# Optimization experiments

Hardware: AMD Instinct MI355X
Metric: run time of the kernel (lower is better)

The kernel has to match this reference:

```python
import jax, jax.numpy as jnp
import numpy as np

B, C, H, W = 16, 64, 64, 64  # z_e shape; C == embedding_dim
K = 1024                     # num_embeddings
COMMITMENT_COST = 0.25
EPS = 1e-5


def setup_inputs() -> dict:
    key = jax.random.key(0)
    k1, k2 = jax.random.split(key)
    z_e = jax.random.normal(k1, (B, C, H, W), dtype=jnp.float32)
    # codebook init ~ U(-1/D, 1/D) as in the torch module
    emb_w = jax.random.uniform(k2, (K, C), dtype=jnp.float32, minval=-1.0 / C, maxval=1.0 / C)
    return {"z_e": z_e, "emb_w": emb_w}


def reference(z_e, emb_w):
    orig_dtype = z_e.dtype
    b, c, h, w = z_e.shape
    z = z_e.astype(jnp.float32)
    # per-channel std over (batch, h, w); computed under no_grad in torch -> stop_gradient
    std = jax.lax.stop_gradient(
        jnp.clip(jnp.std(z, axis=(0, 2, 3), keepdims=True, ddof=1), EPS, None)
    )
    z = z / std                                        # [b,c,h,w]
    zf = z.transpose(0, 2, 3, 1).reshape(-1, c)        # [N, c]
    ew = emb_w.astype(jnp.float32)                     # [K, c]
    # squared euclidean distances: ||z||^2 - 2 z.e + ||e||^2  -> [N, K]
    d = (
        jnp.sum(zf * zf, axis=1, keepdims=True)
        - 2.0 * (zf @ ew.T)
        + jnp.sum(ew * ew, axis=1)
    )
    idx = jnp.argmin(d, axis=1)                        # [N]
    z_q = ew[idx].reshape(b, h, w, c).transpose(0, 3, 1, 2)  # [b,c,h,w]
    z_sg = jax.lax.stop_gradient(z)
    commitment = COMMITMENT_COST * jnp.mean((z_sg - z_q) ** 2)
    codebook = jnp.mean((z_sg - z_q) ** 2)             # eval-mode codebook loss
    vq_loss = commitment + codebook
    z_q_st = (z + jax.lax.stop_gradient(z_q - z)).astype(orig_dtype)
    n_tokens = idx.shape[0]
    counts = jnp.zeros((K,), dtype=jnp.float32).at[idx].add(1.0)
    avg_probs = counts / n_tokens
    perplexity = jnp.exp(-jnp.sum(avg_probs * jnp.log(jnp.clip(avg_probs, 1e-10, None))))
    indices = idx.reshape(b, h, w)
    return z_q_st, vq_loss, perplexity, indices
```

## Files before the change

### kernel.cpp

```cpp
#include <hip/hip_runtime.h>
#include <math.h>
#include <float.h>

#define HW 4096
#define CHW 262144
#define NTOK 65536
#define NELEM 4194304

#define WS_LOSS 0
#define WS_STD  512
#define WS_EE   576
#define WS_E2   1600

#define EPSM 1.5e-4f

typedef __attribute__((ext_vector_type(8))) short bf16x8;
typedef __attribute__((ext_vector_type(4))) float f32x4;

__device__ __forceinline__ unsigned short f2bf(float x) {
  unsigned u = __float_as_uint(x);
  u += 0x7FFFu + ((u >> 16) & 1u);
  return (unsigned short)(u >> 16);
}
__device__ __forceinline__ float bf2f(unsigned short h) {
  return __uint_as_float(((unsigned)h) << 16);
}
__device__ __forceinline__ void gload_lds16(const unsigned short* g, unsigned short* l) {
  __builtin_amdgcn_global_load_lds(
      (const __attribute__((address_space(1))) unsigned int*)g,
      (__attribute__((address_space(3))) unsigned int*)l, 16, 0, 0);
}

__global__ __launch_bounds__(1024) void k_pre(const float* __restrict__ z,
                                              const float* __restrict__ emb,
                                              float* __restrict__ stdv,
                                              unsigned short* __restrict__ e2g,
                                              float* __restrict__ eeg) {
  __shared__ double rs[16], rs2[16];
  int tid = threadIdx.x;
  int blk = blockIdx.x;
  if (blk < 64) {
    int c = blk;
    double s = 0.0, s2 = 0.0;
    const float* base = z + c * HW;
    #pragma unroll 4
    for (int jj = 0; jj < 16; ++jj) {
      int f = tid + (jj << 10);
      int b = f >> 10, off4 = f & 1023;
      float4 v = *(const float4*)(base + (size_t)b * CHW + (off4 << 2));
      s  += (double)v.x + (double)v.y + (double)v.z + (double)v.w;
      s2 += (double)v.x * v.x + (double)v.y * v.y + (double)v.z * v.z + (double)v.w * v.w;
    }
    for (int o = 32; o > 0; o >>= 1) {
      s += __shfl_down(s, o, 64);
      s2 += __shfl_down(s2, o, 64);
    }
    int wv = tid >> 6, ln = tid & 63;
    if (ln == 0) { rs[wv] = s; rs2[wv] = s2; }
    __syncthreads();
    if (tid == 0) {
      double S = 0.0, S2 = 0.0;
      #pragma unroll
      for (int w = 0; w < 16; ++w) { S += rs[w]; S2 += rs2[w]; }
      const double N = (double)NTOK;
      double var = (S2 - S * S / N) / (N - 1.0);
      float sd = (float)sqrt(var);
      stdv[c] = fmaxf(sd, 1e-5f);
    }
  } else {
    int ct = blk - 64;
    int k0 = ct << 6;
    int code = tid >> 4, c4 = tid & 15;
    float4 v = *(const float4*)(emb + (size_t)((k0 + code) << 6) + (c4 << 2));
    unsigned short h0 = f2bf(v.x), h1 = f2bf(v.y), h2 = f2bf(v.z), h3 = f2bf(v.w);
    unsigned short l0 = f2bf(v.x - bf2f(h0)), l1 = f2bf(v.y - bf2f(h1));
    unsigned short l2 = f2bf(v.z - bf2f(h2)), l3 = f2bf(v.w - bf2f(h3));
    int jL = (c4 >> 1) & 3;
    int e = (c4 & 1) << 2;
    int cH = code >> 4, cL = code & 15;
    size_t base = (size_t)ct * 8192 + cH * 512 + jL * 128 + cL * 8 + e;
    int jHh = c4 >> 3;
    *(uint2*)(e2g + base + (size_t)jHh * 2048) =
        make_uint2((unsigned)h0 | ((unsigned)h1 << 16), (unsigned)h2 | ((unsigned)h3 << 16));
    *(uint2*)(e2g + base + (size_t)(2 + jHh) * 2048) =
        make_uint2((unsigned)l0 | ((unsigned)l1 << 16), (unsigned)l2 | ((unsigned)l3 << 16));
    if (tid < 64) {
      const float* er = emb + (size_t)((k0 + tid) << 6);
      float s = 0.f;
      #pragma unroll
      for (int c = 0; c < 64; ++c) s = fmaf(er[c], er[c], s);
      eeg[k0 + tid] = s;
    }
  }
}

__global__ __launch_bounds__(256, 2) void k_vq(
    const float* __restrict__ z_e, const float* __restrict__ emb,
    const float* __restrict__ stdv, const float* __restrict__ eeg,
    const unsigned short* __restrict__ e2g,
    float* __restrict__ out_zq, float* __restrict__ out_idx,
    float* __restrict__ loss_part) {
  __shared__ unsigned short A2[16384];
  __shared__ unsigned short B2[16384];
  float* mbd = (float*)A2;
  float* msec = (float*)A2 + 256;
  int*   mbk = (int*)A2 + 512;
  int*   skf = (int*)A2 + 768;
  int*   ambList = (int*)A2 + 896;
  int*   ambN = (int*)A2 + 1024;
  float* sred = (float*)A2 + 1028;
  float* zf   = (float*)A2 + 1040;
  float* fbd4 = (float*)A2 + 1104;
  int*   fbk4 = (int*)A2 + 1108;

  int tid = threadIdx.x;
  int lane = tid & 63;
  int wv = tid >> 6;
  int blk = blockIdx.x;
  int b = blk >> 5;
  int s0 = (blk & 31) << 7;

  {
    int tok = tid >> 1, half = tid & 1;
    const float* zsrc = z_e + (size_t)b * CHW + (size_t)(half << 5) * HW + s0 + tok;
    unsigned hw_[16], lw_[16];
    #pragma unroll
    for (int cc = 0; cc < 32; ++cc) {
      float v = zsrc[(size_t)cc * HW] / stdv[(half << 5) + cc];
      unsigned short h = f2bf(v);
      unsigned short l = f2bf(v - bf2f(h));
      if (cc & 1) { hw_[cc >> 1] |= ((unsigned)h) << 16; lw_[cc >> 1] |= ((unsigned)l) << 16; }
      else        { hw_[cc >> 1] = h;                    lw_[cc >> 1] = l; }
    }
    int tH = tok >> 4, tL = tok & 15;
    int base = tH * 512 + tL * 8;
    #pragma unroll
    for (int jj = 0; jj < 4; ++jj) {
      *(uint4*)(A2 + half * 4096 + base + jj * 128) =
          make_uint4(hw_[4 * jj], hw_[4 * jj + 1], hw_[4 * jj + 2], hw_[4 * jj + 3]);
      *(uint4*)(A2 + (2 + half) * 4096 + base + jj * 128) =
          make_uint4(lw_[4 * jj], lw_[4 * jj + 1], lw_[4 * jj + 2], lw_[4 * jj + 3]);
    }
  }

  int quad = lane >> 4, l15 = lane & 15;
  int wt = wv >> 1, wc = wv & 1;

  float bd[16], sec[16];
  int bk[16];
  #pragma unroll
  for (int i = 0; i < 16; ++i) { bd[i] = FLT_MAX; sec[i] = FLT_MAX; bk[i] = 0; }

  {
    const unsigned short* gsrc = e2g + wv * 512 + (lane << 3);
    unsigned short* ldst = B2 + wv * 512;
    #pragma unroll
    for (int rr = 0; rr < 4; ++rr)
      gload_lds16(gsrc + rr * 2048, ldst + rr * 2048);
  }

  const int aJH[8] = {0, 1, 2, 3, 0, 1, 2, 3};
  const int bJH[8] = {0, 1, 0, 1, 2, 3, 2, 3};

  for (int ct = 0; ct < 16; ++ct) {
    __syncthreads();
    const unsigned short* bb = B2 + (ct & 1) * 8192;
    if (ct < 15) {
      const unsigned short* gsrc = e2g + (size_t)(ct + 1) * 8192 + wv * 512 + (lane << 3);
      unsigned short* ldst = B2 + ((ct + 1) & 1) * 8192 + wv * 512;
      #pragma unroll
      for (int rr = 0; rr < 4; ++rr)
        gload_lds16(gsrc + rr * 2048, ldst + rr * 2048);
    }

    f32x4 acc[4][2];
    #pragma unroll
    for (int mt = 0; mt < 4; ++mt) { acc[mt][0] = (f32x4)(0.f); acc[mt][1] = (f32x4)(0.f); }

    #pragma unroll
    for (int s = 0; s < 8; ++s) {
      bf16x8 af[4], bfr[2];
      #pragma unroll
      for (int mt = 0; mt < 4; ++mt)
        af[mt] = *(const bf16x8*)(A2 + aJH[s] * 4096 + ((wt << 2) + mt) * 512 + quad * 128 + l15 * 8);
      #pragma unroll
      for (int nt = 0; nt < 2; ++nt)
        bfr[nt] = *(const bf16x8*)(bb + bJH[s] * 2048 + ((wc << 1) + nt) * 512 + quad * 128 + l15 * 8);
      #pragma unroll
      for (int mt = 0; mt < 4; ++mt)
        #pragma unroll
        for (int nt = 0; nt < 2; ++nt)
          acc[mt][nt] = __builtin_amdgcn_mfma_f32_16x16x32_bf16(af[mt], bfr[nt], acc[mt][nt], 0, 0, 0);
    }

    #pragma unroll
    for (int nt = 0; nt < 2; ++nt) {
      int kcode = (ct << 6) + ((wc << 1) + nt) * 16 + l15;
      float eev = eeg[kcode];
      #pragma unroll
      for (int mt = 0; mt < 4; ++mt) {
        #pragma unroll
        for (int r = 0; r < 4; ++r) {
          float sv = fmaf(-2.0f, acc[mt][nt][r], eev);
          int slot = (mt << 2) + r;
          if (sv < bd[slot]) { sec[slot] = bd[slot]; bd[slot] = sv; bk[slot] = kcode; }
          else if (sv < sec[slot]) { sec[slot] = sv; }
        }
      }
    }
  }
  __syncthreads();

  #pragma unroll
  for (int m = 1; m <= 8; m <<= 1) {
    #pragma unroll
    for (int slot = 0; slot < 16; ++slot) {
      float obd = __shfl_xor(bd[slot], m, 64);
      int   obk = __shfl_xor(bk[slot], m, 64);
      float osec = __shfl_xor(sec[slot], m, 64);
      if (obd < bd[slot] || (obd == bd[slot] && obk < bk[slot])) {
        sec[slot] = fminf(bd[slot], osec); bd[slot] = obd; bk[slot] = obk;
      } else {
        sec[slot] = fminf(sec[slot], obd);
      }
    }
  }
  if (tid == 0) *ambN = 0;
  if (l15 == 0) {
    #pragma unroll
    for (int mt = 0; mt < 4; ++mt)
      #pragma unroll
      for (int r = 0; r < 4; ++r) {
        int t = (wt << 6) + (mt << 4) + (quad << 2) + r;
        int slot = (mt << 2) + r;
        mbd[(wc << 7) + t] = bd[slot]; mbk[(wc << 7) + t] = bk[slot]; msec[(wc << 7) + t] = sec[slot];
      }
  }
  __syncthreads();

  if (tid < 128) {
    float b0 = mbd[tid], b1 = mbd[128 + tid];
    int k0 = mbk[tid], k1 = mbk[128 + tid];
    float fbd, fsec; int fbk;
    if (b1 < b0 || (b1 == b0 && k1 < k0)) { fbd = b1; fbk = k1; fsec = fminf(b0, msec[128 + tid]); }
    else                                  { fbd = b0; fbk = k0; fsec = fminf(msec[tid], b1); }
    skf[tid] = fbk;
    if (fsec - fbd <= EPSM) { int p = atomicAdd(ambN, 1); ambList[p] = tid; }
  }
  __syncthreads();

  {
    int na = *ambN;
    for (int i = 0; i < na; ++i) {
      int t = ambList[i];
      if (tid < 64) zf[tid] = z_e[(size_t)b * CHW + (size_t)tid * HW + s0 + t] / stdv[tid];
      __syncthreads();
      const float4* zf4 = (const float4*)zf;
      const float* er0 = emb + ((size_t)(tid << 2) << 6);
      float zz = 0.f;
      float dot[4] = {0.f, 0.f, 0.f, 0.f};
      #pragma unroll
      for (int c4 = 0; c4 < 16; ++c4) {
        float4 zv = zf4[c4];
        zz = fmaf(zv.x, zv.x, zz); zz = fmaf(zv.y, zv.y, zz);
        zz = fmaf(zv.z, zv.z, zz); zz = fmaf(zv.w, zv.w, zz);
        #pragma unroll
        for (int j = 0; j < 4; ++j) {
          float4 ev = *(const float4*)(er0 + (j << 6) + (c4 << 2));
          dot[j] = fmaf(ev.x, zv.x, dot[j]);
          dot[j] = fmaf(ev.y, zv.y, dot[j]);
          dot[j] = fmaf(ev.z, zv.z, dot[j]);
          dot[j] = fmaf(ev.w, zv.w, dot[j]);
        }
      }
      float bdl = FLT_MAX; int bkl = 0;
      #pragma unroll
      for (int j = 0; j < 4; ++j) {
        float dd = (zz - 2.0f * dot[j]) + eeg[(tid << 2) + j];
        if (dd < bdl) { bdl = dd; bkl = (tid << 2) + j; }
      }
      #pragma unroll
      for (int m = 1; m <= 32; m <<= 1) {
        float od = __shfl_xor(bdl, m, 64);
        int   ok = __shfl_xor(bkl, m, 64);
        if (od < bdl || (od == bdl && ok < bkl)) { bdl = od; bkl = ok; }
      }
      if (lane == 0) { fbd4[wv] = bdl; fbk4[wv] = bkl; }
      __syncthreads();
      if (tid == 0) {
        float bb2 = fbd4[0]; int kk2 = fbk4[0];
        #pragma unroll
        for (int w = 1; w < 4; ++w)
          if (fbd4[w] < bb2 || (fbd4[w] == bb2 && fbk4[w] < kk2)) { bb2 = fbd4[w]; kk2 = fbk4[w]; }
        skf[t] = kk2;
      }
      __syncthreads();
    }
  }
  __syncthreads();

  if (tid < 128) out_idx[(blk << 7) + tid] = (float)skf[tid];

  {
    int t = tid & 127;
    int ch = tid >> 7;
    int kq = skf[t];
    const float* eq = emb + ((size_t)kq << 6) + (ch << 5);
    const float* zb2 = z_e + (size_t)b * CHW + s0 + t;
    float* ob = out_zq + (size_t)b * CHW + s0 + t;
    float lsum = 0.f;
    #pragma unroll
    for (int jj = 0; jj < 32; ++jj) {
      int c = (ch << 5) + jj;
      float zv = zb2[(size_t)c * HW] / stdv[c];
      float e = eq[jj];
      float df = zv - e;
      lsum = fmaf(df, df, lsum);
      ob[(size_t)c * HW] = zv + (e - zv);
    }
    for (int o = 32; o > 0; o >>= 1) lsum += __shfl_down(lsum, o, 64);
    if (lane == 0) sred[wv] = lsum;
  }
  __syncthreads();
  if (tid == 0) loss_part[blk] = sred[0] + sred[1] + sred[2] + sred[3];
}

__global__ __launch_bounds__(1024) void k_post(const float* __restrict__ loss_part,
                                               const float* __restrict__ out_idx,
                                               float* __restrict__ out_scalars) {
  __shared__ int hist[1024];
  __shared__ double rl[16], rh[16];
  int tid = threadIdx.x;
  hist[tid] = 0;
  __syncthreads();
  const float2* idx2 = (const float2*)out_idx;
  #pragma unroll
  for (int jj = 0; jj < 32; ++jj) {
    float2 v = idx2[tid + (jj << 10)];
    atomicAdd(&hist[(int)v.x], 1);
    atomicAdd(&hist[(int)v.y], 1);
  }
  __syncthreads();
  double ls = 0.0;
  if (tid < 512) ls = (double)loss_part[tid];
  float p = (float)hist[tid] * (1.0f / 65536.0f);
  float lg = logf(fmaxf(p, 1e-10f));
  double hs = (double)(p * lg);
  for (int o = 32; o > 0; o >>= 1) {
    ls += __shfl_down(ls, o, 64);
    hs += __shfl_down(hs, o, 64);
  }
  int wv = tid >> 6, ln = tid & 63;
  if (ln == 0) { rl[wv] = ls; rh[wv] = hs; }
  __syncthreads();
  if (tid == 0) {
    double L = 0.0, Hn = 0.0;
    #pragma unroll
    for (int w = 0; w < 16; ++w) { L += rl[w]; Hn += rh[w]; }
    float m = (float)(L / (double)NELEM);
    out_scalars[0] = 0.25f * m + m;
    out_scalars[1] = expf((float)(-Hn));
  }
}

extern "C" void kernel_launch(void* const* d_in, const int* in_sizes, int n_in,
                              void* d_out, int out_size, void* d_ws, size_t ws_size,
                              hipStream_t stream) {
  const float* z_e = (const float*)d_in[0];
  const float* emb = (const float*)d_in[1];
  float* ws = (float*)d_ws;
  float* loss_part = ws + WS_LOSS;
  float* stdv = ws + WS_STD;
  float* eeg = ws + WS_EE;
  unsigned short* e2g = (unsigned short*)(ws + WS_E2);

  float* out = (float*)d_out;
  float* out_zq = out;
  float* out_scalars = out + NELEM;
  float* out_idx = out + NELEM + 2;

  k_pre<<<80, 1024, 0, stream>>>(z_e, emb, stdv, e2g, eeg);
  k_vq<<<512, 256, 0, stream>>>(z_e, emb, stdv, eeg, e2g, out_zq, out_idx, loss_part);
  k_post<<<1, 1024, 0, stream>>>(loss_part, out_idx, out_scalars);
}
```

Before: 225.5 us.

## Fuse post kernel via last-block reduction, track top-3 and add cheap pairwise refinement

Removes the separate k_post launch: each k_vq block increments an atomic counter after writing its loss partial, and the last block builds the histogram and computes the scalars. The argmin tracking now keeps the best two codes and the third distance, so near-tie tokens whose third candidate is clearly worse get a per-thread fp32 check of just two codes instead of the serial full 1024-code block-wide rescan. A-fragments are hoisted into registers once, the per-tile leading barrier is moved to the end of the tile, and the ambiguity threshold is tightened. The costs are higher register pressure from the cached fragments and top-3 state, and a serial tail in the last block.

```diff
diff --git a/kernel.cpp b/kernel.cpp
--- a/kernel.cpp
+++ b/kernel.cpp
@@ -11,8 +11,9 @@
 #define WS_STD  512
 #define WS_EE   576
 #define WS_E2   1600
-
-#define EPSM 1.5e-4f
+#define WS_DONE 132672
+
+#define EPSM 1.0e-4f
 
 typedef __attribute__((ext_vector_type(8))) short bf16x8;
 typedef __attribute__((ext_vector_type(4))) float f32x4;
@@ -35,10 +36,12 @@
                                               const float* __restrict__ emb,
                                               float* __restrict__ stdv,
                                               unsigned short* __restrict__ e2g,
-                                              float* __restrict__ eeg) {
+                                              float* __restrict__ eeg,
+                                              int* __restrict__ done) {
   __shared__ double rs[16], rs2[16];
   int tid = threadIdx.x;
   int blk = blockIdx.x;
+  if (blk == 0 && tid == 0) *done = 0;
   if (blk < 64) {
     int c = blk;
     double s = 0.0, s2 = 0.0;
@@ -99,19 +102,28 @@
     const float* __restrict__ stdv, const float* __restrict__ eeg,
     const unsigned short* __restrict__ e2g,
     float* __restrict__ out_zq, float* __restrict__ out_idx,
-    float* __restrict__ loss_part) {
+    float* __restrict__ loss_part, int* __restrict__ done,
+    float* __restrict__ out_scalars) {
   __shared__ unsigned short A2[16384];
   __shared__ unsigned short B2[16384];
-  float* mbd = (float*)A2;
-  float* msec = (float*)A2 + 256;
-  int*   mbk = (int*)A2 + 512;
-  int*   skf = (int*)A2 + 768;
-  int*   ambList = (int*)A2 + 896;
-  int*   ambN = (int*)A2 + 1024;
-  float* sred = (float*)A2 + 1028;
-  float* zf   = (float*)A2 + 1040;
-  float* fbd4 = (float*)A2 + 1104;
-  int*   fbk4 = (int*)A2 + 1108;
+  __shared__ double rl[4], rh[4];
+  __shared__ int lastFlag;
+  float* hs1 = (float*)A2;
+  float* hs2 = (float*)A2 + 256;
+  float* hs3 = (float*)A2 + 512;
+  int*   hk1 = (int*)A2 + 768;
+  int*   hk2 = (int*)A2 + 1024;
+  int*   skf = (int*)A2 + 1280;
+  int*   mk2f = (int*)A2 + 1408;
+  int*   pairL = (int*)A2 + 1536;
+  int*   fullL = (int*)A2 + 1664;
+  int*   cntB = (int*)A2 + 1792;
+  int*   cntC = (int*)A2 + 1793;
+  float* sred = (float*)A2 + 1796;
+  float* zf   = (float*)A2 + 1800;
+  float* fbd4 = (float*)A2 + 1864;
+  int*   fbk4 = (int*)A2 + 1868;
+  int*   hist = (int*)A2 + 1872;
 
   int tid = threadIdx.x;
   int lane = tid & 63;
@@ -146,11 +158,6 @@
   int quad = lane >> 4, l15 = lane & 15;
   int wt = wv >> 1, wc = wv & 1;
 
-  float bd[16], sec[16];
-  int bk[16];
-  #pragma unroll
-  for (int i = 0; i < 16; ++i) { bd[i] = FLT_MAX; sec[i] = FLT_MAX; bk[i] = 0; }
-
   {
     const unsigned short* gsrc = e2g + wv * 512 + (lane << 3);
     unsigned short* ldst = B2 + wv * 512;
@@ -158,12 +165,25 @@
     for (int rr = 0; rr < 4; ++rr)
       gload_lds16(gsrc + rr * 2048, ldst + rr * 2048);
   }
+  __syncthreads();
+
+  bf16x8 afc[4][4];
+  #pragma unroll
+  for (int j = 0; j < 4; ++j)
+    #pragma unroll
+    for (int mt = 0; mt < 4; ++mt)
+      afc[j][mt] = *(const bf16x8*)(A2 + j * 4096 + ((wt << 2) + mt) * 512 + quad * 128 + l15 * 8);
+
+  float ts1[16], ts2[16], ts3[16];
+  int tk1[16], tk2[16];
+  #pragma unroll
+  for (int i = 0; i < 16; ++i) { ts1[i] = FLT_MAX; ts2[i] = FLT_MAX; ts3[i] = FLT_MAX; tk1[i] = 0; tk2[i] = 0; }
 
   const int aJH[8] = {0, 1, 2, 3, 0, 1, 2, 3};
   const int bJH[8] = {0, 1, 0, 1, 2, 3, 2, 3};
 
+  #pragma unroll 1
   for (int ct = 0; ct < 16; ++ct) {
-    __syncthreads();
     const unsigned short* bb = B2 + (ct & 1) * 8192;
     if (ct < 15) {
       const unsigned short* gsrc = e2g + (size_t)(ct + 1) * 8192 + wv * 512 + (lane << 3);
@@ -172,6 +192,8 @@
       for (int rr = 0; rr < 4; ++rr)
         gload_lds16(gsrc + rr * 2048, ldst + rr * 2048);
     }
+    float ee0 = eeg[(ct << 6) + (wc << 5) + l15];
+    float ee1 = eeg[(ct << 6) + (wc << 5) + 16 + l15];
 
     f32x4 acc[4][2];
     #pragma unroll
@@ -179,10 +201,7 @@
 
     #pragma unroll
     for (int s = 0; s < 8; ++s) {
-      bf16x8 af[4], bfr[2];
-      #pragma unroll
-      for (int mt = 0; mt < 4; ++mt)
-        af[mt] = *(const bf16x8*)(A2 + aJH[s] * 4096 + ((wt << 2) + mt) * 512 + quad * 128 + l15 * 8);
+      bf16x8 bfr[2];
       #pragma unroll
       for (int nt = 0; nt < 2; ++nt)
         bfr[nt] = *(const bf16x8*)(bb + bJH[s] * 2048 + ((wc << 1) + nt) * 512 + quad * 128 + l15 * 8);
@@ -190,112 +209,153 @@
       for (int mt = 0; mt < 4; ++mt)
         #pragma unroll
         for (int nt = 0; nt < 2; ++nt)
-          acc[mt][nt] = __builtin_amdgcn_mfma_f32_16x16x32_bf16(af[mt], bfr[nt], acc[mt][nt], 0, 0, 0);
+          acc[mt][nt] = __builtin_amdgcn_mfma_f32_16x16x32_bf16(afc[aJH[s]][mt], bfr[nt], acc[mt][nt], 0, 0, 0);
     }
 
     #pragma unroll
     for (int nt = 0; nt < 2; ++nt) {
-      int kcode = (ct << 6) + ((wc << 1) + nt) * 16 + l15;
-      float eev = eeg[kcode];
+      int kc = (ct << 6) + (wc << 5) + (nt << 4) + l15;
+      float eev = nt ? ee1 : ee0;
       #pragma unroll
       for (int mt = 0; mt < 4; ++mt) {
         #pragma unroll
         for (int r = 0; r < 4; ++r) {
           float sv = fmaf(-2.0f, acc[mt][nt][r], eev);
-          int slot = (mt << 2) + r;
-          if (sv < bd[slot]) { sec[slot] = bd[slot]; bd[slot] = sv; bk[slot] = kcode; }
-          else if (sv < sec[slot]) { sec[slot] = sv; }
+          int sl = (mt << 2) + r;
+          bool lt1 = sv < ts1[sl];
+          bool lt2 = sv < ts2[sl];
+          bool lt3 = sv < ts3[sl];
+          ts3[sl] = lt2 ? ts2[sl] : (lt3 ? sv : ts3[sl]);
+          tk2[sl] = lt1 ? tk1[sl] : (lt2 ? kc : tk2[sl]);
+          ts2[sl] = lt1 ? ts1[sl] : (lt2 ? sv : ts2[sl]);
+          tk1[sl] = lt1 ? kc : tk1[sl];
+          ts1[sl] = lt1 ? sv : ts1[sl];
         }
       }
     }
+    if (ct < 15) __syncthreads();
   }
   __syncthreads();
 
   #pragma unroll
   for (int m = 1; m <= 8; m <<= 1) {
     #pragma unroll
-    for (int slot = 0; slot < 16; ++slot) {
-      float obd = __shfl_xor(bd[slot], m, 64);
-      int   obk = __shfl_xor(bk[slot], m, 64);
-      float osec = __shfl_xor(sec[slot], m, 64);
-      if (obd < bd[slot] || (obd == bd[slot] && obk < bk[slot])) {
-        sec[slot] = fminf(bd[slot], osec); bd[slot] = obd; bk[slot] = obk;
-      } else {
-        sec[slot] = fminf(sec[slot], obd);
-      }
-    }
-  }
-  if (tid == 0) *ambN = 0;
+    for (int sl = 0; sl < 16; ++sl) {
+      float ob1 = __shfl_xor(ts1[sl], m, 64); int oq1 = __shfl_xor(tk1[sl], m, 64);
+      float ob2 = __shfl_xor(ts2[sl], m, 64); int oq2 = __shfl_xor(tk2[sl], m, 64);
+      float ob3 = __shfl_xor(ts3[sl], m, 64);
+      bool t1 = (ts1[sl] < ob1) || (ts1[sl] == ob1 && tk1[sl] < oq1);
+      float o1 = t1 ? ts1[sl] : ob1; int ok1 = t1 ? tk1[sl] : oq1;
+      float aH = t1 ? ts2[sl] : ts1[sl]; int aHk = t1 ? tk2[sl] : tk1[sl]; float aH2 = t1 ? ts3[sl] : ts2[sl];
+      float bH = t1 ? ob1 : ob2;         int bHk = t1 ? oq1 : oq2;         float bH2 = t1 ? ob2 : ob3;
+      bool t2 = (aH < bH) || (aH == bH && aHk < bHk);
+      float o2 = t2 ? aH : bH; int ok2 = t2 ? aHk : bHk;
+      float aI = t2 ? aH2 : aH;
+      float bI = t2 ? bH : bH2;
+      ts1[sl] = o1; tk1[sl] = ok1; ts2[sl] = o2; tk2[sl] = ok2; ts3[sl] = fminf(aI, bI);
+    }
+  }
+  if (tid == 0) { *cntB = 0; *cntC = 0; }
   if (l15 == 0) {
     #pragma unroll
     for (int mt = 0; mt < 4; ++mt)
       #pragma unroll
       for (int r = 0; r < 4; ++r) {
         int t = (wt << 6) + (mt << 4) + (quad << 2) + r;
-        int slot = (mt << 2) + r;
-        mbd[(wc << 7) + t] = bd[slot]; mbk[(wc << 7) + t] = bk[slot]; msec[(wc << 7) + t] = sec[slot];
+        int sl = (mt << 2) + r;
+        hs1[(wc << 7) + t] = ts1[sl]; hs2[(wc << 7) + t] = ts2[sl]; hs3[(wc << 7) + t] = ts3[sl];
+        hk1[(wc << 7) + t] = tk1[sl]; hk2[(wc << 7) + t] = tk2[sl];
       }
   }
   __syncthreads();
 
   if (tid < 128) {
-    float b0 = mbd[tid], b1 = mbd[128 + tid];
-    int k0 = mbk[tid], k1 = mbk[128 + tid];
-    float fbd, fsec; int fbk;
-    if (b1 < b0 || (b1 == b0 && k1 < k0)) { fbd = b1; fbk = k1; fsec = fminf(b0, msec[128 + tid]); }
-    else                                  { fbd = b0; fbk = k0; fsec = fminf(msec[tid], b1); }
-    skf[tid] = fbk;
-    if (fsec - fbd <= EPSM) { int p = atomicAdd(ambN, 1); ambList[p] = tid; }
-  }
-  __syncthreads();
-
-  {
-    int na = *ambN;
-    for (int i = 0; i < na; ++i) {
-      int t = ambList[i];
-      if (tid < 64) zf[tid] = z_e[(size_t)b * CHW + (size_t)tid * HW + s0 + t] / stdv[tid];
-      __syncthreads();
-      const float4* zf4 = (const float4*)zf;
-      const float* er0 = emb + ((size_t)(tid << 2) << 6);
-      float zz = 0.f;
-      float dot[4] = {0.f, 0.f, 0.f, 0.f};
-      #pragma unroll
-      for (int c4 = 0; c4 < 16; ++c4) {
-        float4 zv = zf4[c4];
-        zz = fmaf(zv.x, zv.x, zz); zz = fmaf(zv.y, zv.y, zz);
-        zz = fmaf(zv.z, zv.z, zz); zz = fmaf(zv.w, zv.w, zz);
-        #pragma unroll
-        for (int j = 0; j < 4; ++j) {
-          float4 ev = *(const float4*)(er0 + (j << 6) + (c4 << 2));
-          dot[j] = fmaf(ev.x, zv.x, dot[j]);
-          dot[j] = fmaf(ev.y, zv.y, dot[j]);
-          dot[j] = fmaf(ev.z, zv.z, dot[j]);
-          dot[j] = fmaf(ev.w, zv.w, dot[j]);
-        }
+    float a1 = hs1[tid], a2 = hs2[tid], a3 = hs3[tid];
+    int e1 = hk1[tid], e2 = hk2[tid];
+    float b1 = hs1[128 + tid], b2 = hs2[128 + tid], b3 = hs3[128 + tid];
+    int f1 = hk1[128 + tid], f2 = hk2[128 + tid];
+    bool t1 = (a1 < b1) || (a1 == b1 && e1 < f1);
+    float o1 = t1 ? a1 : b1; int ok1 = t1 ? e1 : f1;
+    float aH = t1 ? a2 : a1; int aHk = t1 ? e2 : e1; float aH2 = t1 ? a3 : a2;
+    float bH = t1 ? b1 : b2; int bHk = t1 ? f1 : f2; float bH2 = t1 ? b2 : b3;
+    bool t2 = (aH < bH) || (aH == bH && aHk < bHk);
+    float o2 = t2 ? aH : bH; int ok2 = t2 ? aHk : bHk;
+    float o3 = fminf(t2 ? aH2 : aH, t2 ? bH : bH2);
+    skf[tid] = ok1;
+    mk2f[tid] = ok2;
+    if (o2 - o1 <= EPSM) {
+      if (o3 - o1 > EPSM) { int p = atomicAdd(cntB, 1); pairL[p] = tid; }
+      else                { int p = atomicAdd(cntC, 1); fullL[p] = tid; }
+    }
+  }
+  __syncthreads();
+
+  int nB = *cntB, nC = *cntC;
+
+  if (tid < nB) {
+    int t = pairL[tid];
+    int ka = skf[t], kb = mk2f[t];
+    const float* za = z_e + (size_t)b * CHW + s0 + t;
+    const float* ea = emb + ((size_t)ka << 6);
+    const float* ebp = emb + ((size_t)kb << 6);
+    float zz = 0.f, da = 0.f, db = 0.f;
+    #pragma unroll
+    for (int c = 0; c < 64; ++c) {
+      float zv = za[(size_t)c * HW] / stdv[c];
+      zz = fmaf(zv, zv, zz);
+      da = fmaf(ea[c], zv, da);
+      db = fmaf(ebp[c], zv, db);
+    }
+    float d1 = (zz - 2.0f * da) + eeg[ka];
+    float d2 = (zz - 2.0f * db) + eeg[kb];
+    if (d2 < d1 || (d2 == d1 && kb < ka)) skf[t] = kb;
+  }
+  __syncthreads();
+
+  for (int i = 0; i < nC; ++i) {
+    int t = fullL[i];
+    if (tid < 64) zf[tid] = z_e[(size_t)b * CHW + (size_t)tid * HW + s0 + t] / stdv[tid];
+    __syncthreads();
+    const float4* zf4 = (const float4*)zf;
+    const float* er0 = emb + ((size_t)(tid << 2) << 6);
+    float zz = 0.f;
+    float dot[4] = {0.f, 0.f, 0.f, 0.f};
+    #pragma unroll
+    for (int c4 = 0; c4 < 16; ++c4) {
+      float4 zv = zf4[c4];
+      zz = fmaf(zv.x, zv.x, zz); zz = fmaf(zv.y, zv.y, zz);
+      zz = fmaf(zv.z, zv.z, zz); zz = fmaf(zv.w, zv.w, zz);
+      #pragma unroll
+      for (int j = 0; j < 4; ++j) {
+        float4 ev = *(const float4*)(er0 + (j << 6) + (c4 << 2));
+        dot[j] = fmaf(ev.x, zv.x, dot[j]);
+        dot[j] = fmaf(ev.y, zv.y, dot[j]);
+        dot[j] = fmaf(ev.z, zv.z, dot[j]);
+        dot[j] = fmaf(ev.w, zv.w, dot[j]);
       }
-      float bdl = FLT_MAX; int bkl = 0;
-      #pragma unroll
-      for (int j = 0; j < 4; ++j) {
-        float dd = (zz - 2.0f * dot[j]) + eeg[(tid << 2) + j];
-        if (dd < bdl) { bdl = dd; bkl = (tid << 2) + j; }
-      }
-      #pragma unroll
-      for (int m = 1; m <= 32; m <<= 1) {
-        float od = __shfl_xor(bdl, m, 64);
-        int   ok = __shfl_xor(bkl, m, 64);
-        if (od < bdl || (od == bdl && ok < bkl)) { bdl = od; bkl = ok; }
-      }
-      if (lane == 0) { fbd4[wv] = bdl; fbk4[wv] = bkl; }
-      __syncthreads();
-      if (tid == 0) {
-        float bb2 = fbd4[0]; int kk2 = fbk4[0];
-        #pragma unroll
-        for (int w = 1; w < 4; ++w)
-          if (fbd4[w] < bb2 || (fbd4[w] == bb2 && fbk4[w] < kk2)) { bb2 = fbd4[w]; kk2 = fbk4[w]; }
-        skf[t] = kk2;
-      }
-      __syncthreads();
-    }
+    }
+    float bdl = FLT_MAX; int bkl = 0;
+    #pragma unroll
+    for (int j = 0; j < 4; ++j) {
+      float dd = (zz - 2.0f * dot[j]) + eeg[(tid << 2) + j];
+      if (dd < bdl) { bdl = dd; bkl = (tid << 2) + j; }
+    }
+    #pragma unroll
+    for (int m = 1; m <= 32; m <<= 1) {
+      float od = __shfl_xor(bdl, m, 64);
+      int   ok = __shfl_xor(bkl, m, 64);
+      if (od < bdl || (od == bdl && ok < bkl)) { bdl = od; bkl = ok; }
+    }
+    if (lane == 0) { fbd4[wv] = bdl; fbk4[wv] = bkl; }
+    __syncthreads();
+    if (tid == 0) {
+      float bb2 = fbd4[0]; int kk2 = fbk4[0];
+      #pragma unroll
+      for (int w = 1; w < 4; ++w)
+        if (fbd4[w] < bb2 || (fbd4[w] == bb2 && fbk4[w] < kk2)) { bb2 = fbd4[w]; kk2 = fbk4[w]; }
+      skf[t] = kk2;
+    }
+    __syncthreads();
   }
   __syncthreads();
 
@@ -322,41 +382,45 @@
     if (lane == 0) sred[wv] = lsum;
   }
   __syncthreads();
-  if (tid == 0) loss_part[blk] = sred[0] + sred[1] + sred[2] + sred[3];
-}
-
-__global__ __launch_bounds__(1024) void k_post(const float* __restrict__ loss_part,
-                                               const float* __restrict__ out_idx,
-                                               float* __restrict__ out_scalars) {
-  __shared__ int hist[1024];
-  __shared__ double rl[16], rh[16];
-  int tid = threadIdx.x;
-  hist[tid] = 0;
-  __syncthreads();
-  const float2* idx2 = (const float2*)out_idx;
+
+  if (tid == 0) {
+    loss_part[blk] = sred[0] + sred[1] + sred[2] + sred[3];
+    __threadfence();
+    int prev = atomicAdd(done, 1);
+    lastFlag = (prev == 511);
+  }
+  __syncthreads();
+  if (!lastFlag) return;
+
   #pragma unroll
-  for (int jj = 0; jj < 32; ++jj) {
-    float2 v = idx2[tid + (jj << 10)];
-    atomicAdd(&hist[(int)v.x], 1);
-    atomicAdd(&hist[(int)v.y], 1);
-  }
-  __syncthreads();
-  double ls = 0.0;
-  if (tid < 512) ls = (double)loss_part[tid];
-  float p = (float)hist[tid] * (1.0f / 65536.0f);
-  float lg = logf(fmaxf(p, 1e-10f));
-  double hs = (double)(p * lg);
+  for (int jj = 0; jj < 4; ++jj) hist[tid + (jj << 8)] = 0;
+  __syncthreads();
+  {
+    const float2* idx2 = (const float2*)out_idx;
+    for (int i = tid; i < NTOK / 2; i += 256) {
+      float2 v = idx2[i];
+      atomicAdd(&hist[(int)v.x], 1);
+      atomicAdd(&hist[(int)v.y], 1);
+    }
+  }
+  __syncthreads();
+  double ls = (double)loss_part[tid] + (double)loss_part[tid + 256];
+  double hsum = 0.0;
+  #pragma unroll
+  for (int jj = 0; jj < 4; ++jj) {
+    float p = (float)hist[tid + (jj << 8)] * (1.0f / 65536.0f);
+    float lg = logf(fmaxf(p, 1e-10f));
+    hsum += (double)(p * lg);
+  }
   for (int o = 32; o > 0; o >>= 1) {
     ls += __shfl_down(ls, o, 64);
-    hs += __shfl_down(hs, o, 64);
-  }
-  int wv = tid >> 6, ln = tid & 63;
-  if (ln == 0) { rl[wv] = ls; rh[wv] = hs; }
+    hsum += __shfl_down(hsum, o, 64);
+  }
+  if (lane == 0) { rl[wv] = ls; rh[wv] = hsum; }
   __syncthreads();
   if (tid == 0) {
-    double L = 0.0, Hn = 0.0;
-    #pragma unroll
-    for (int w = 0; w < 16; ++w) { L += rl[w]; Hn += rh[w]; }
+    double L = rl[0] + rl[1] + rl[2] + rl[3];
+    double Hn = rh[0] + rh[1] + rh[2] + rh[3];
     float m = (float)(L / (double)NELEM);
     out_scalars[0] = 0.25f * m + m;
     out_scalars[1] = expf((float)(-Hn));
@@ -373,13 +437,14 @@
   float* stdv = ws + WS_STD;
   float* eeg = ws + WS_EE;
   unsigned short* e2g = (unsigned short*)(ws + WS_E2);
+  int* done = (int*)(ws + WS_DONE);
 
   float* out = (float*)d_out;
   float* out_zq = out;
   float* out_scalars = out + NELEM;
   float* out_idx = out + NELEM + 2;
 
-  k_pre<<<80, 1024, 0, stream>>>(z_e, emb, stdv, e2g, eeg);
-  k_vq<<<512, 256, 0, stream>>>(z_e, emb, stdv, eeg, e2g, out_zq, out_idx, loss_part);
-  k_post<<<1, 1024, 0, stream>>>(loss_part, out_idx, out_scalars);
-}
+  k_pre<<<80, 1024, 0, stream>>>(z_e, emb, stdv, e2g, eeg, done);
+  k_vq<<<512, 256, 0, stream>>>(z_e, emb, stdv, eeg, e2g, out_zq, out_idx,
+                                loss_part, done, out_scalars);
+}
```

Result: faster. 191.9 us (-14.9%).
